# Performance work log

Measured on AMD Instinct MI355X. Metric: run time of the kernel, lower is better.

Reference implementation:

```python
import jax, jax.numpy as jnp
import numpy as np

B, T, H = 4, 4096, 2048
G_EPS = 0.5
LN_EPS = 1e-5
INIT_STD = 0.02


def setup_inputs() -> dict:
    key = jax.random.key(0)
    ks = jax.random.split(key, 4)
    return {
        "hidden_states": jax.random.normal(ks[0], (B, T, H), jnp.float32),
        "W_z": jax.random.normal(ks[1], (H, H), jnp.float32) * INIT_STD,
        "b_z": jnp.zeros((H,), jnp.float32),
        "W_h": jax.random.normal(ks[2], (H, H), jnp.float32) * INIT_STD,
        "b_h": jnp.zeros((H,), jnp.float32),
        "ln_w": jnp.ones((H,), jnp.float32),
        "ln_b": jnp.zeros((H,), jnp.float32),
        "h0": jax.random.normal(ks[3], (H,), jnp.float32) * INIT_STD,
    }


def _g_log(x):
    # torch.where(x >= 0, log(relu(x) + g_eps), -softplus(-x))
    return jnp.where(x >= 0, jnp.log(jax.nn.relu(x) + G_EPS), -jax.nn.softplus(-x))


def reference(hidden_states, W_z, b_z, W_h, b_h, ln_w, ln_b, h0):
    Bc, Tc, Hc = hidden_states.shape
    k = hidden_states @ W_z.T + b_z                      # [B,T,H]
    log_z = -jax.nn.softplus(-k)                         # log sigmoid(k)
    log_coeffs = -jax.nn.softplus(k)                     # log(1 - sigmoid(k))
    log_tilde_h = _g_log(hidden_states @ W_h.T + b_h)    # [B,T,H]
    log_h0 = jnp.broadcast_to(_g_log(h0), (Bc, 1, Hc))
    log_values = jnp.concatenate([log_h0, log_z + log_tilde_h], axis=1)  # [B,T+1,H]
    # NOTE: faithful to source: cumsum over the LAST (hidden) dim, then pad one
    # zero row at the front of the time dim (F.pad(..., (0,0,1,0))).
    a_star = jnp.pad(jnp.cumsum(log_coeffs, axis=-1), ((0, 0), (1, 0), (0, 0)))  # [B,T+1,H]
    log_h = a_star + jax.lax.cumlogsumexp(log_values - a_star, axis=1)
    # global mean / unbiased std normalization, as in source
    log_h = (log_h - log_h.mean()) / jnp.std(log_h, ddof=1)
    h = jnp.exp(log_h)[:, 1:, :]                         # drop the h0 step
    # residual + LayerNorm (dropout is identity in eval)
    x = h + hidden_states
    mu = x.mean(axis=-1, keepdims=True)
    var = x.var(axis=-1, keepdims=True)
    return (x - mu) * jax.lax.rsqrt(var + LN_EPS) * ln_w + ln_b
```

## Files before the change

kernel.cpp:

```cpp
#include <hip/hip_runtime.h>
#include <stdint.h>

constexpr int NB = 4;
constexpr int NT = 4096;
constexpr int NH = 2048;
constexpr int MROWS = NB * NT;
constexpr int TP1 = NT + 1;
constexpr int CH2 = 17;
constexpr int NCH2 = 241;

typedef unsigned short u16;
typedef __bf16 bf16x8 __attribute__((ext_vector_type(8)));
typedef float f32x4 __attribute__((ext_vector_type(4)));
typedef unsigned short u16x8 __attribute__((ext_vector_type(8)));
typedef _Float16 h16x8 __attribute__((ext_vector_type(8)));
typedef u16x8 __attribute__((may_alias)) u16x8_a;
typedef h16x8 __attribute__((may_alias)) h16x8_a;
typedef float4 __attribute__((may_alias)) float4_a;

__device__ __forceinline__ u16 f2bf(float f) {
  unsigned int u = __float_as_uint(f);
  return (u16)((u + 0x7fffu + ((u >> 16) & 1u)) >> 16);
}
__device__ __forceinline__ float bf2f(u16 v) {
  return __uint_as_float(((unsigned int)v) << 16);
}
__device__ __forceinline__ float spf_(float x) {
  return fmaxf(x, 0.f) + __logf(1.f + __expf(-fabsf(x)));
}
__device__ __forceinline__ float glogf_(float x) {
  return (x >= 0.f) ? __logf(x + 0.5f) : -spf_(-x);
}
__device__ __forceinline__ void gld16(const void* g, void* l) {
  __builtin_amdgcn_global_load_lds((const __attribute__((address_space(1))) void*)g,
                                   (__attribute__((address_space(3))) void*)l, 16, 0, 0);
}
__device__ __forceinline__ void ld8(const float* p, float* r) {
  float4 a = *(const float4_a*)p, b = *(const float4_a*)(p + 4);
  r[0] = a.x; r[1] = a.y; r[2] = a.z; r[3] = a.w;
  r[4] = b.x; r[5] = b.y; r[6] = b.z; r[7] = b.w;
}
__device__ __forceinline__ void st8(float* p, const float* r) {
  *(float4_a*)p       = make_float4(r[0], r[1], r[2], r[3]);
  *(float4_a*)(p + 4) = make_float4(r[4], r[5], r[6], r[7]);
}
__device__ __forceinline__ void lsecomb(float& M, float& S, float Mo, float So) {
  const float Mn = fmaxf(M, Mo);
  float Sn = S * __expf(M - Mn) + So * __expf(Mo - Mn);
  if (Mn == -INFINITY) Sn = 0.f;
  M = Mn; S = Sn;
}

__global__ __launch_bounds__(256) void cvt_all(
    const float* __restrict__ hs, const float* __restrict__ Wz,
    const float* __restrict__ Wh, u16* __restrict__ hsb,
    u16* __restrict__ wzb, u16* __restrict__ whb) {
  const int s0 = MROWS * NH / 8;
  const int s1 = s0 + NH * NH / 8;
  const int s2 = s1 + NH * NH / 8;
  int i = blockIdx.x * 256 + threadIdx.x;
  if (i >= s2) return;
  const float* in; u16* out; int j;
  if (i < s0)      { in = hs; out = hsb; j = i; }
  else if (i < s1) { in = Wz; out = wzb; j = i - s0; }
  else             { in = Wh; out = whb; j = i - s1; }
  const float4* p = (const float4*)in;
  float4 a = p[2 * (size_t)j], b = p[2 * (size_t)j + 1];
  u16x8 o;
  o[0] = f2bf(a.x); o[1] = f2bf(a.y); o[2] = f2bf(a.z); o[3] = f2bf(a.w);
  o[4] = f2bf(b.x); o[5] = f2bf(b.y); o[6] = f2bf(b.z); o[7] = f2bf(b.w);
  *(u16x8*)(out + (size_t)j * 8) = o;
}

__global__ __launch_bounds__(256, 3) void gemm_bt(
    const u16* __restrict__ A,
    const u16* __restrict__ Bz, const u16* __restrict__ Bh,
    const float* __restrict__ bz, const float* __restrict__ bh,
    u16* __restrict__ KU) {
  const u16* Bm  = blockIdx.y ? Bh : Bz;
  const float* bias = blockIdx.y ? bh : bz;
  u16* Cw = KU + (blockIdx.y ? 2048 : 0);

  const int bid = blockIdx.x;
  const int wg = (bid & 7) * 256 + (bid >> 3);
  const int bx = wg & 15;
  const int by = wg >> 4;
  const int row0 = by << 7, col0 = bx << 7;

  __shared__ u16 ldsA[128 * 64];
  __shared__ u16 ldsB[128 * 64];

  const int tid = threadIdx.x;
  const int lane = tid & 63;
  const int wv = tid >> 6;
  const int wr = (wv >> 1) << 6;
  const int wc = (wv & 1) << 6;

  const int srow = lane >> 3;
  const int sslot = ((lane & 7) ^ srow) << 3;
  const int xsw = (lane & 7) << 3;
  const int q8 = (lane >> 4) << 3;
  const int f15 = lane & 15;

  f32x4 acc[4][4] = {};

  for (int k0 = 0; k0 < NH; k0 += 64) {
    if (k0) __syncthreads();
#pragma unroll
    for (int i = 0; i < 4; ++i) {
      const int r = i * 32 + wv * 8 + srow;
      const size_t gcol = (size_t)(k0 + sslot);
      gld16(A  + (size_t)(row0 + r) * NH + gcol, &ldsA[(size_t)(i * 256 + wv * 64) * 8]);
      gld16(Bm + (size_t)(col0 + r) * NH + gcol, &ldsB[(size_t)(i * 256 + wv * 64) * 8]);
    }
    __syncthreads();
#pragma unroll
    for (int ks = 0; ks < 2; ++ks) {
      const int cphys = ((ks << 5) | q8) ^ xsw;
      bf16x8 af[4], bfr[4];
#pragma unroll
      for (int m = 0; m < 4; ++m)
        af[m] = *(const bf16x8*)&ldsA[(wr + m * 16 + f15) * 64 + cphys];
#pragma unroll
      for (int n = 0; n < 4; ++n)
        bfr[n] = *(const bf16x8*)&ldsB[(wc + n * 16 + f15) * 64 + cphys];
#pragma unroll
      for (int m = 0; m < 4; ++m)
#pragma unroll
        for (int n = 0; n < 4; ++n)
          acc[m][n] = __builtin_amdgcn_mfma_f32_16x16x32_bf16(af[m], bfr[n], acc[m][n], 0, 0, 0);
    }
  }

  const int fr = lane & 15, fq = lane >> 4;
#pragma unroll
  for (int n = 0; n < 4; ++n) {
    const int col = col0 + wc + n * 16 + fr;
    const float bv = bias[col];
#pragma unroll
    for (int m = 0; m < 4; ++m) {
#pragma unroll
      for (int v = 0; v < 4; ++v) {
        const int row = row0 + wr + m * 16 + fq * 4 + v;
        Cw[(size_t)row * 4096 + col] = f2bf(acc[m][n][v] + bv);
      }
    }
  }
}

__device__ __forceinline__ void row_pointwise(const char* KU, size_t row,
                                              int tid, float* lc, float* lv) {
  const size_t rb = row * 8192;
  u16x8 kv = *(const u16x8_a*)(KU + rb + tid * 16);
  u16x8 uv = *(const u16x8_a*)(KU + rb + 4096 + tid * 16);
#pragma unroll
  for (int e = 0; e < 8; ++e) {
    const float k = bf2f(kv[e]);
    const float L = __logf(1.f + __expf(-fabsf(k)));
    lc[e] = -fmaxf(k, 0.f) - L;
    lv[e] = fminf(k, 0.f) - L + glogf_(bf2f(uv[e]));
  }
}

__global__ __launch_bounds__(256) void carry_pass(
    const char* __restrict__ KU, float* __restrict__ cm, float* __restrict__ cs,
    const float* __restrict__ h0) {
  const int ch = blockIdx.x;
  const int b = blockIdx.y;
  const int tid = threadIdx.x;
  const int lane = tid & 63, wvx = tid >> 6;
  const int t0 = ch * CH2;
  const int t1 = (t0 + CH2 < TP1) ? (t0 + CH2) : TP1;

  float m8[8], s8[8];
#pragma unroll
  for (int e = 0; e < 8; ++e) { m8[e] = -INFINITY; s8[e] = 0.f; }

  __shared__ float wsum[2][4];

  float lc[8], lv[8];
  {
    const int tf = (t0 < 1) ? 1 : t0;
    if (tf < t1) row_pointwise(KU, (size_t)b * NT + (tf - 1), tid, lc, lv);
  }

  for (int tt = t0; tt < t1; ++tt) {
    if (tt == 0) {
#pragma unroll
      for (int e = 0; e < 8; ++e) {
        const float x = glogf_(h0[tid * 8 + e]);
        m8[e] = x; s8[e] = 1.f;
      }
      continue;
    }
    float nlc[8], nlv[8];
    const bool pf = (tt + 1 < t1);
    if (pf) row_pointwise(KU, (size_t)b * NT + tt, tid, nlc, nlv);

    float cum[8], run = 0.f;
#pragma unroll
    for (int e = 0; e < 8; ++e) { run += lc[e]; cum[e] = run; }
    float v = run;
#pragma unroll
    for (int d = 1; d < 64; d <<= 1) {
      float o = __shfl_up(v, d, 64);
      if (lane >= d) v += o;
    }
    const int par = tt & 1;
    if (lane == 63) wsum[par][wvx] = v;
    __syncthreads();
    float base = v - run;
#pragma unroll
    for (int w = 0; w < 4; ++w)
      if (w < wvx) base += wsum[par][w];

#pragma unroll
    for (int e = 0; e < 8; ++e) {
      const float x = lv[e] - (base + cum[e]);
      const float nm = fmaxf(m8[e], x);
      s8[e] = s8[e] * __expf(m8[e] - nm) + __expf(x - nm);
      m8[e] = nm;
    }
    if (pf) {
#pragma unroll
      for (int e = 0; e < 8; ++e) { lc[e] = nlc[e]; lv[e] = nlv[e]; }
    }
  }
  const size_t co = ((size_t)ch * NB + b) * NH + tid * 8;
  st8(cm + co, m8);
  st8(cs + co, s8);
}

__global__ __launch_bounds__(256) void carryscan(float* __restrict__ cm,
                                                 float* __restrict__ cs) {
  const int wvx = threadIdx.x >> 6, lane = threadIdx.x & 63;
  const int c = blockIdx.x * 4 + wvx;
  const int b = c >> 11;
  const int hh = c & (NH - 1);
  float Cm = -INFINITY, Cs = 0.f;
#pragma unroll
  for (int s = 0; s < 4; ++s) {
    const int idx = s * 64 + lane;
    const bool val = (idx < NCH2);
    size_t o = 0;
    float M = -INFINITY, S = 0.f;
    if (val) {
      o = ((size_t)idx * NB + b) * NH + hh;
      M = cm[o]; S = cs[o];
    }
#pragma unroll
    for (int d = 1; d < 64; d <<= 1) {
      const float Mo = __shfl_up(M, d, 64);
      const float So = __shfl_up(S, d, 64);
      if (lane >= d) lsecomb(M, S, Mo, So);
    }
    float Me = __shfl_up(M, 1, 64);
    float Se = __shfl_up(S, 1, 64);
    if (lane == 0) { Me = -INFINITY; Se = 0.f; }
    float Om = Cm, Os = Cs;
    lsecomb(Om, Os, Me, Se);
    if (val) { cm[o] = Om; cs[o] = Os; }
    const float Mt = __shfl(M, 63, 64);
    const float St = __shfl(S, 63, 64);
    lsecomb(Cm, Cs, Mt, St);
  }
}

template <int HLH>
__global__ __launch_bounds__(256) void scan_final(
    const char* __restrict__ KU, float* __restrict__ LH32,
    _Float16* __restrict__ LH16,
    const float* __restrict__ cm, const float* __restrict__ cs,
    const float* __restrict__ h0, double* __restrict__ sums) {
  const int ch = blockIdx.x;
  const int b = blockIdx.y;
  const int tid = threadIdx.x;
  const int lane = tid & 63, wvx = tid >> 6;
  const int t0 = ch * CH2;
  const int t1 = (t0 + CH2 < TP1) ? (t0 + CH2) : TP1;

  float m8[8], s8[8];
  {
    const size_t co = ((size_t)ch * NB + b) * NH + tid * 8;
    ld8(cm + co, m8);
    ld8(cs + co, s8);
  }

  __shared__ float wsum[2][4];
  double s1 = 0.0, s2 = 0.0;

  float lc[8], lv[8];
  {
    const int tf = (t0 < 1) ? 1 : t0;
    if (tf < t1) row_pointwise(KU, (size_t)b * NT + (tf - 1), tid, lc, lv);
  }

  for (int tt = t0; tt < t1; ++tt) {
    if (tt == 0) {
#pragma unroll
      for (int e = 0; e < 8; ++e) {
        const float x = glogf_(h0[tid * 8 + e]);
        m8[e] = x; s8[e] = 1.f;
        s1 += (double)x;
        s2 += (double)x * (double)x;
      }
      continue;
    }
    float nlc[8], nlv[8];
    const bool pf = (tt + 1 < t1);
    if (pf) row_pointwise(KU, (size_t)b * NT + tt, tid, nlc, nlv);

    float cum[8], run = 0.f;
#pragma unroll
    for (int e = 0; e < 8; ++e) { run += lc[e]; cum[e] = run; }
    float v = run;
#pragma unroll
    for (int d = 1; d < 64; d <<= 1) {
      float o = __shfl_up(v, d, 64);
      if (lane >= d) v += o;
    }
    const int par = tt & 1;
    if (lane == 63) wsum[par][wvx] = v;
    __syncthreads();
    float base = v - run;
#pragma unroll
    for (int w = 0; w < 4; ++w)
      if (w < wvx) base += wsum[par][w];

    float lh8[8];
#pragma unroll
    for (int e = 0; e < 8; ++e) {
      const float as = base + cum[e];
      const float x = lv[e] - as;
      const float nm = fmaxf(m8[e], x);
      s8[e] = s8[e] * __expf(m8[e] - nm) + __expf(x - nm);
      m8[e] = nm;
      const float lh = as + nm + __logf(s8[e]);
      lh8[e] = lh;
      s1 += (double)lh;
      s2 += (double)lh * (double)lh;
    }
    const size_t row = (size_t)b * NT + (tt - 1);
    if (HLH) {
      h16x8 hv;
#pragma unroll
      for (int e = 0; e < 8; ++e) hv[e] = (_Float16)lh8[e];
      *(h16x8_a*)(LH16 + row * NH + tid * 8) = hv;
    } else {
      st8(LH32 + row * NH + tid * 8, lh8);
    }
    if (pf) {
#pragma unroll
      for (int e = 0; e < 8; ++e) { lc[e] = nlc[e]; lv[e] = nlv[e]; }
    }
  }
  double v1 = s1, v2 = s2;
#pragma unroll
  for (int d = 32; d; d >>= 1) {
    v1 += __shfl_down(v1, d, 64);
    v2 += __shfl_down(v2, d, 64);
  }
  __shared__ double dr1[4], dr2[4];
  if (lane == 0) { dr1[wvx] = v1; dr2[wvx] = v2; }
  __syncthreads();
  if (tid == 0) {
    atomicAdd(&sums[0], dr1[0] + dr1[1] + dr1[2] + dr1[3]);
    atomicAdd(&sums[1], dr2[0] + dr2[1] + dr2[2] + dr2[3]);
  }
}

__global__ void finalize_stats(const double* __restrict__ sums,
                               float* __restrict__ stats) {
  const double S = sums[0], S2 = sums[1];
  const double N = (double)NB * (double)TP1 * (double)NH;
  const double mu = S / N;
  const double var = (S2 - S * S / N) / (N - 1.0);
  stats[0] = (float)mu;
  stats[1] = (float)(1.0 / sqrt(var));
}

template <int HLH>
__global__ __launch_bounds__(256) void final_ln(
    float* __restrict__ OUT, const float* __restrict__ LH32,
    const _Float16* __restrict__ LH16, const u16* __restrict__ hsb,
    const float* __restrict__ lnw, const float* __restrict__ lnb,
    const float* __restrict__ stats) {
  const int tid = threadIdx.x;
  const size_t off = (size_t)blockIdx.x * NH + tid * 8;
  const float mu_g = stats[0], isd = stats[1];

  float lh[8], av[8];
  if (HLH) {
    h16x8 hv = *(const h16x8_a*)(LH16 + off);
#pragma unroll
    for (int e = 0; e < 8; ++e) lh[e] = (float)hv[e];
  } else {
    ld8(LH32 + off, lh);
  }
  {
    u16x8 hv = *(const u16x8_a*)(hsb + off);
#pragma unroll
    for (int e = 0; e < 8; ++e) av[e] = bf2f(hv[e]);
  }
  float x[8];
  float s = 0.f, q = 0.f;
#pragma unroll
  for (int e = 0; e < 8; ++e) {
    x[e] = __expf((lh[e] - mu_g) * isd) + av[e];
    s += x[e];
    q += x[e] * x[e];
  }
#pragma unroll
  for (int d = 32; d; d >>= 1) {
    s += __shfl_down(s, d, 64);
    q += __shfl_down(q, d, 64);
  }
  __shared__ float r1[4], r2[4];
  const int lane = tid & 63, wvx = tid >> 6;
  if (lane == 0) { r1[wvx] = s; r2[wvx] = q; }
  __syncthreads();
  const float st = r1[0] + r1[1] + r1[2] + r1[3];
  const float qt = r2[0] + r2[1] + r2[2] + r2[3];
  const float mean = st * (1.0f / NH);
  const float var = qt * (1.0f / NH) - mean * mean;
  const float rstd = rsqrtf(var + 1e-5f);

  float wv8[8], bv8[8];
  ld8(lnw + tid * 8, wv8);
  ld8(lnb + tid * 8, bv8);
  float o[8];
#pragma unroll
  for (int e = 0; e < 8; ++e)
    o[e] = (x[e] - mean) * rstd * wv8[e] + bv8[e];
  st8(OUT + off, o);
}

extern "C" void kernel_launch(void* const* d_in, const int* in_sizes, int n_in,
                              void* d_out, int out_size, void* d_ws, size_t ws_size,
                              hipStream_t stream) {
  (void)in_sizes; (void)n_in; (void)out_size;
  const float* hs  = (const float*)d_in[0];
  const float* Wz  = (const float*)d_in[1];
  const float* bz  = (const float*)d_in[2];
  const float* Wh  = (const float*)d_in[3];
  const float* bh  = (const float*)d_in[4];
  const float* lnw = (const float*)d_in[5];
  const float* lnb = (const float*)d_in[6];
  const float* h0  = (const float*)d_in[7];
  float* out = (float*)d_out;

  char* w0 = (char*)d_ws;
  char* w = w0;
  u16* hsb   = (u16*)w;  w += (size_t)MROWS * NH * 2;
  u16* wzb   = (u16*)w;  w += (size_t)NH * NH * 2;
  u16* whb   = (u16*)w;  w += (size_t)NH * NH * 2;
  char* KU   = w;        w += (size_t)MROWS * 8192;
  double* sums = (double*)w; w += 16;
  float* stats = (float*)w;  w += 64;
  _Float16* LH16 = (_Float16*)w;
  const size_t need_half = (size_t)(w - w0) + (size_t)MROWS * NH * 2;
  const bool use_half = (ws_size >= need_half);
  float* cm_ = (float*)wzb;
  float* cs_ = cm_ + (size_t)NCH2 * NB * NH;

  hipMemsetAsync(sums, 0, 16, stream);

  {
    const int tot8 = MROWS * NH / 8 + 2 * (NH * NH / 8);
    cvt_all<<<dim3((tot8 + 255) / 256), 256, 0, stream>>>(hs, Wz, Wh, hsb, wzb, whb);
  }

  gemm_bt<<<dim3((MROWS / 128) * (NH / 128), 2), 256, 0, stream>>>(
      hsb, wzb, whb, bz, bh, (u16*)KU);

  carry_pass<<<dim3(NCH2, NB), 256, 0, stream>>>(KU, cm_, cs_, h0);

  carryscan<<<dim3(NB * NH / 4), 256, 0, stream>>>(cm_, cs_);

  if (use_half)
    scan_final<1><<<dim3(NCH2, NB), 256, 0, stream>>>(KU, out, LH16, cm_, cs_, h0, sums);
  else
    scan_final<0><<<dim3(NCH2, NB), 256, 0, stream>>>(KU, out, LH16, cm_, cs_, h0, sums);
  finalize_stats<<<1, 1, 0, stream>>>(sums, stats);

  if (use_half)
    final_ln<1><<<dim3(MROWS), 256, 0, stream>>>(out, out, LH16, hsb, lnw, lnb, stats);
  else
    final_ln<0><<<dim3(MROWS), 256, 0, stream>>>(out, out, LH16, hsb, lnw, lnb, stats);
}
```

Measured before the change: 599.1 us.

## Replace strided per-column carry scan with coalesced three-phase group scan

The old carry scan assigned one wavefront per (batch, hidden) column and read chunk carries with a stride of NB*NH, which gave uncoalesced memory access. The new version gives each thread one column and runs three kernels: a reduction over groups of 16 chunks, an exclusive scan across the group totals, and an apply pass that writes the exclusive prefix for each chunk. Adjacent threads now read adjacent addresses. In exchange it adds two kernel launches, a sequential serial loop per thread, and extra workspace that shifts where LH16 starts.

```diff
diff --git a/kernel.cpp b/kernel.cpp
--- a/kernel.cpp
+++ b/kernel.cpp
@@ -8,6 +8,9 @@
 constexpr int TP1 = NT + 1;
 constexpr int CH2 = 17;
 constexpr int NCH2 = 241;
+constexpr int GSZ = 16;
+constexpr int NGRP = (NCH2 + GSZ - 1) / GSZ;
+constexpr int NCOL = NB * NH;
 
 typedef unsigned short u16;
 typedef __bf16 bf16x8 __attribute__((ext_vector_type(8)));
@@ -231,38 +234,48 @@
   st8(cs + co, s8);
 }
 
-__global__ __launch_bounds__(256) void carryscan(float* __restrict__ cm,
-                                                 float* __restrict__ cs) {
-  const int wvx = threadIdx.x >> 6, lane = threadIdx.x & 63;
-  const int c = blockIdx.x * 4 + wvx;
-  const int b = c >> 11;
-  const int hh = c & (NH - 1);
-  float Cm = -INFINITY, Cs = 0.f;
-#pragma unroll
-  for (int s = 0; s < 4; ++s) {
-    const int idx = s * 64 + lane;
-    const bool val = (idx < NCH2);
-    size_t o = 0;
-    float M = -INFINITY, S = 0.f;
-    if (val) {
-      o = ((size_t)idx * NB + b) * NH + hh;
-      M = cm[o]; S = cs[o];
-    }
-#pragma unroll
-    for (int d = 1; d < 64; d <<= 1) {
-      const float Mo = __shfl_up(M, d, 64);
-      const float So = __shfl_up(S, d, 64);
-      if (lane >= d) lsecomb(M, S, Mo, So);
-    }
-    float Me = __shfl_up(M, 1, 64);
-    float Se = __shfl_up(S, 1, 64);
-    if (lane == 0) { Me = -INFINITY; Se = 0.f; }
-    float Om = Cm, Os = Cs;
-    lsecomb(Om, Os, Me, Se);
-    if (val) { cm[o] = Om; cs[o] = Os; }
-    const float Mt = __shfl(M, 63, 64);
-    const float St = __shfl(S, 63, 64);
-    lsecomb(Cm, Cs, Mt, St);
+__global__ __launch_bounds__(256) void carry_groupred(
+    const float* __restrict__ cm, const float* __restrict__ cs,
+    float* __restrict__ gm, float* __restrict__ gs) {
+  const int c = blockIdx.x * 256 + threadIdx.x;
+  const int g = blockIdx.y;
+  const int ch0 = g * GSZ;
+  const int ch1 = (ch0 + GSZ < NCH2) ? (ch0 + GSZ) : NCH2;
+  float M = -INFINITY, S = 0.f;
+  for (int ch = ch0; ch < ch1; ++ch) {
+    const size_t o = (size_t)ch * NCOL + c;
+    lsecomb(M, S, cm[o], cs[o]);
+  }
+  gm[(size_t)g * NCOL + c] = M;
+  gs[(size_t)g * NCOL + c] = S;
+}
+
+__global__ __launch_bounds__(256) void carry_groupscan(float* __restrict__ gm,
+                                                       float* __restrict__ gs) {
+  const int c = blockIdx.x * 256 + threadIdx.x;
+  float M = -INFINITY, S = 0.f;
+  for (int g = 0; g < NGRP; ++g) {
+    const size_t o = (size_t)g * NCOL + c;
+    const float m2 = gm[o], s2 = gs[o];
+    gm[o] = M; gs[o] = S;
+    lsecomb(M, S, m2, s2);
+  }
+}
+
+__global__ __launch_bounds__(256) void carry_apply(
+    float* __restrict__ cm, float* __restrict__ cs,
+    const float* __restrict__ gm, const float* __restrict__ gs) {
+  const int c = blockIdx.x * 256 + threadIdx.x;
+  const int g = blockIdx.y;
+  const int ch0 = g * GSZ;
+  const int ch1 = (ch0 + GSZ < NCH2) ? (ch0 + GSZ) : NCH2;
+  float M = gm[(size_t)g * NCOL + c];
+  float S = gs[(size_t)g * NCOL + c];
+  for (int ch = ch0; ch < ch1; ++ch) {
+    const size_t o = (size_t)ch * NCOL + c;
+    const float m2 = cm[o], s2 = cs[o];
+    cm[o] = M; cs[o] = S;
+    lsecomb(M, S, m2, s2);
   }
 }
 
@@ -457,11 +470,13 @@
   char* KU   = w;        w += (size_t)MROWS * 8192;
   double* sums = (double*)w; w += 16;
   float* stats = (float*)w;  w += 64;
+  float* gm_ = (float*)w;    w += (size_t)NGRP * NCOL * 4;
+  float* gs_ = (float*)w;    w += (size_t)NGRP * NCOL * 4;
   _Float16* LH16 = (_Float16*)w;
   const size_t need_half = (size_t)(w - w0) + (size_t)MROWS * NH * 2;
   const bool use_half = (ws_size >= need_half);
   float* cm_ = (float*)wzb;
-  float* cs_ = cm_ + (size_t)NCH2 * NB * NH;
+  float* cs_ = cm_ + (size_t)NCH2 * NCOL;
 
   hipMemsetAsync(sums, 0, 16, stream);
 
@@ -475,7 +490,9 @@
 
   carry_pass<<<dim3(NCH2, NB), 256, 0, stream>>>(KU, cm_, cs_, h0);
 
-  carryscan<<<dim3(NB * NH / 4), 256, 0, stream>>>(cm_, cs_);
+  carry_groupred<<<dim3(NCOL / 256, NGRP), 256, 0, stream>>>(cm_, cs_, gm_, gs_);
+  carry_groupscan<<<dim3(NCOL / 256), 256, 0, stream>>>(gm_, gs_);
+  carry_apply<<<dim3(NCOL / 256, NGRP), 256, 0, stream>>>(cm_, cs_, gm_, gs_);
 
   if (use_half)
     scan_final<1><<<dim3(NCH2, NB), 256, 0, stream>>>(KU, out, LH16, cm_, cs_, h0, sums);
```

Result: faster. 554.5 us (-7.4%).
